# Kernel optimization log

Measured on AMD Instinct MI355X. Metric: run time of the kernel, lower is better.

The kernel has to match this reference:

```python
import jax, jax.numpy as jnp
import numpy as np

B, N, C, H, D, M = 8, 4096, 512, 8, 64, 16
TOPK = 3
TAU = 0.1
DIV_REG = 0.01


def setup_inputs() -> dict:
    key = jax.random.key(0)
    ks = jax.random.split(key, 12)
    w = lambda i, shape: 0.02 * jax.random.normal(ks[i], shape, dtype=jnp.float32)
    return {
        "x": jax.random.normal(ks[0], (B, N, C), dtype=jnp.float32),
        "W_qkv": w(1, (C, 3 * C)),                    # qkv_bias=False
        "W_proj": w(2, (C, C)), "b_proj": jnp.zeros((C,), jnp.float32),
        "W_rspec": w(3, (C, H * M)), "b_rspec": jnp.zeros((H * M,), jnp.float32),
        "W_rspat": w(4, (C, H * M)), "b_rspat": jnp.zeros((H * M,), jnp.float32),
        "K_spec": w(5, (H, M, D)),                    # prototype banks (EMA buffers)
        "K_spat": w(6, (H, M, D)),
        "W_tok": w(7, (D, D)), "b_tok": jnp.zeros((D,), jnp.float32),
        "W_prot": w(8, (D, D)), "b_prot": jnp.zeros((D,), jnp.float32),
    }


def topk_mask_from_logits(logits, k):
    # keep top-k of softmax probs along last axis, renormalize
    vals = jax.lax.top_k(logits, k)[0]
    thresh = vals[..., -1:]
    mask = (logits >= thresh).astype(logits.dtype)
    probs = jax.nn.softmax(logits, axis=-1) * mask
    denom = jnp.maximum(jnp.sum(probs, axis=-1, keepdims=True), 1e-6)
    return probs / denom


def _l2norm(a, eps):
    return a / jnp.maximum(jnp.linalg.norm(a, axis=-1, keepdims=True), eps)


def reference(x, W_qkv, W_proj, b_proj, W_rspec, b_rspec, W_rspat, b_rspat,
              K_spec, K_spat, W_tok, b_tok, W_prot, b_prot):
    # qkv: [B,N,3C] -> q,k,v each [B,H,N,D]
    qkv = (x @ W_qkv).reshape(B, N, 3, H, D).transpose(2, 0, 3, 1, 4)
    q, _k, v = qkv[0], qkv[1], qkv[2]

    # routing logits [B,H,N,M] -> top-k masked probs
    r_spec = topk_mask_from_logits(
        (x @ W_rspec + b_rspec).reshape(B, N, H, M).transpose(0, 2, 1, 3), TOPK)
    r_spat = topk_mask_from_logits(
        (x @ W_rspat + b_rspat).reshape(B, N, H, M).transpose(0, 2, 1, 3), TOPK)

    # effective keys from prototype banks: [B,H,N,D]
    K_eff = (jnp.einsum('bhnm,hmd->bhnd', r_spec, K_spec)
             + jnp.einsum('bhnm,hmd->bhnd', r_spat, K_spat))
    K_norm = jax.nn.softmax(K_eff, axis=-2)          # softmax over tokens N

    # linear attention reorder: context [B,H,D,D], then Q @ context
    context = jnp.einsum('bhnd,bhne->bhde', K_norm, v)
    out = jnp.einsum('bhnd,bhde->bhne', q, context)  # note: scale unused in source
    out = out.transpose(0, 2, 1, 3).reshape(B, N, C) @ W_proj + b_proj

    # ---- contrastive aux loss ----
    t_n = _l2norm(v @ W_tok + b_tok, 1e-12)          # [B,H,N,D]
    p_spec_n = _l2norm(K_spec @ W_prot + b_prot, 1e-12)
    p_spat_n = _l2norm(K_spat @ W_prot + b_prot, 1e-12)
    sim_spec = jnp.einsum('bhnd,hmd->bhnm', t_n, p_spec_n)
    sim_spat = jnp.einsum('bhnd,hmd->bhnm', t_n, p_spat_n)
    pos_spec = jnp.sum(sim_spec * r_spec, axis=-1)
    pos_spat = jnp.sum(sim_spat * r_spat, axis=-1)
    loss_spec = -jnp.mean(pos_spec / TAU - jax.nn.logsumexp(sim_spec / TAU, axis=-1))
    loss_spat = -jnp.mean(pos_spat / TAU - jax.nn.logsumexp(sim_spat / TAU, axis=-1))
    contrastive_loss = 0.5 * (loss_spec + loss_spat)

    def diversity_loss(P):
        h, m, _d = P.shape
        p = P / jnp.maximum(jnp.linalg.norm(P, axis=-1, keepdims=True), 1e-6)
        sim = jnp.einsum('hmd,hnd->hmn', p, p)
        mask = 1.0 - jnp.eye(m, dtype=P.dtype)[None]
        return jnp.sum(sim * mask) / (h * m * (m - 1) + 1e-6)

    diversity = DIV_REG * (diversity_loss(K_spec) + diversity_loss(K_spat))
    return out, contrastive_loss, diversity
```

## Files before the change

kernel.cpp:

```cpp
#include <hip/hip_runtime.h>
#include <math.h>

#define B_ 8
#define N_ 4096
#define C_ 512
#define H_ 8
#define D_ 64
#define M_ 16
#define BN_TOK (B_*N_)
#define TAU_ 0.1f

typedef short s8v __attribute__((ext_vector_type(8)));
typedef float f4v __attribute__((ext_vector_type(4)));
typedef unsigned short u16;

__device__ __forceinline__ float wave_reduce_sum(float v){
  #pragma unroll
  for (int o = 32; o > 0; o >>= 1) v += __shfl_xor(v, o);
  return v;
}

__device__ __forceinline__ unsigned short f2b(float f){
  unsigned int u = __float_as_uint(f);
  u += 0x7fffu + ((u >> 16) & 1u);
  return (unsigned short)(u >> 16);
}

__device__ __forceinline__ float b2f(u16 b){
  return __uint_as_float(((unsigned int)b) << 16);
}

__device__ __forceinline__ s8v pack8(const float* f){
  s8v r;
  #pragma unroll
  for (int e = 0; e < 8; ++e) r[e] = (short)f2b(f[e]);
  return r;
}

__device__ __forceinline__ void gload16(const u16* g, u16* l){
  __builtin_amdgcn_global_load_lds(
      (const __attribute__((address_space(1))) unsigned int*)g,
      (__attribute__((address_space(3))) unsigned int*)l, 16, 0, 0);
}

__global__ __launch_bounds__(256) void prep_all(const float* __restrict__ x, u16* __restrict__ xb,
                                                const float* __restrict__ W_qkv,
                                                const float* __restrict__ W_rspec,
                                                const float* __restrict__ W_rspat,
                                                const float* __restrict__ W_proj,
                                                u16* __restrict__ Wt_qv,
                                                u16* __restrict__ Wt_r,
                                                u16* __restrict__ Wt_p){
  const int bid = blockIdx.x;
  if (bid < 1024) {
    const int n8 = (BN_TOK*C_)/8;
    for (int i = bid * 256 + threadIdx.x; i < n8; i += 1024*256) {
      const float4* p = (const float4*)(x + (size_t)i * 8);
      float4 a = p[0], b = p[1];
      float f[8] = {a.x,a.y,a.z,a.w,b.x,b.y,b.z,b.w};
      *(s8v*)(xb + (size_t)i * 8) = pack8(f);
    }
    return;
  }
  const int r = bid - 1024, k = threadIdx.x;
  const float* src; int ld, coff, n; u16* dst;
  if (r < 512)       { src = W_qkv;   ld = 1536; coff = 0;    n = r;        dst = Wt_qv; }
  else if (r < 1024) { src = W_qkv;   ld = 1536; coff = 1024; n = r - 512;  dst = Wt_qv + 512*512; }
  else if (r < 1152) { src = W_rspec; ld = 128;  coff = 0;    n = r - 1024; dst = Wt_r; }
  else if (r < 1280) { src = W_rspat; ld = 128;  coff = 0;    n = r - 1152; dst = Wt_r + 128*512; }
  else               { src = W_proj;  ld = 512;  coff = 0;    n = r - 1280; dst = Wt_p; }
  dst[(size_t)n*512 + k]       = f2b(src[(size_t)k*ld + coff + n]);
  dst[(size_t)n*512 + k + 256] = f2b(src[(size_t)(k+256)*ld + coff + n]);
}

template<bool OUT_BF16>
__global__ __launch_bounds__(256) void gemm_bt(const u16* __restrict__ A,
                                               const u16* __restrict__ Bt,
                                               const float* __restrict__ bias,
                                               void* __restrict__ C,
                                               int K, int lda, int ldc, int bt_bstride) {
  __shared__ __align__(16) u16 Asm[2][128*32];
  __shared__ __align__(16) u16 Bsm[2][128*32];
  const int tid = threadIdx.x;
  const int lane = tid & 63, w = tid >> 6;
  const int bm = blockIdx.x * 128, bn = blockIdx.y * 128;

  const int lrow = lane >> 2;
  const int kch  = ((lane & 3) ^ ((lane >> 3) & 3)) << 3;

  const u16* Btb = Bt + (size_t)(bm >> 12) * bt_bstride;
  const u16* Ag0 = A   + (size_t)(bm + w*16 + lrow) * lda + kch;
  const u16* Ag1 = Ag0 + (size_t)64 * lda;
  const u16* Bg0 = Btb + (size_t)(bn + w*16 + lrow) * K + kch;
  const u16* Bg1 = Bg0 + (size_t)64 * K;
  const int l0 = (w*16)*32, l1 = (w*16+64)*32;

  const int lm = lane & 15, lg = lane >> 4;
  const int w0 = (w >> 1) * 64, c0 = (w & 1) * 64;
  const int xs = (lg ^ ((lm >> 1) & 3)) << 3;

  f4v acc[4][4];
  #pragma unroll
  for (int i = 0; i < 4; ++i)
    #pragma unroll
    for (int j = 0; j < 4; ++j) acc[i][j] = (f4v){0.f,0.f,0.f,0.f};

  gload16(Ag0, &Asm[0][l0]);
  gload16(Ag1, &Asm[0][l1]);
  gload16(Bg0, &Bsm[0][l0]);
  gload16(Bg1, &Bsm[0][l1]);
  __syncthreads();

  int cur = 0;
  for (int k0 = 0; k0 < K; k0 += 32) {
    const int nxt = cur ^ 1;
    if (k0 + 32 < K) {
      gload16(Ag0 + k0 + 32, &Asm[nxt][l0]);
      gload16(Ag1 + k0 + 32, &Asm[nxt][l1]);
      gload16(Bg0 + k0 + 32, &Bsm[nxt][l0]);
      gload16(Bg1 + k0 + 32, &Bsm[nxt][l1]);
    }
    s8v af[4], bf_[4];
    #pragma unroll
    for (int i = 0; i < 4; ++i) af[i]  = *(const s8v*)&Asm[cur][(w0 + 16*i + lm)*32 + xs];
    #pragma unroll
    for (int j = 0; j < 4; ++j) bf_[j] = *(const s8v*)&Bsm[cur][(c0 + 16*j + lm)*32 + xs];
    #pragma unroll
    for (int i = 0; i < 4; ++i)
      #pragma unroll
      for (int j = 0; j < 4; ++j)
        acc[i][j] = __builtin_amdgcn_mfma_f32_16x16x32_bf16(af[i], bf_[j], acc[i][j], 0, 0, 0);
    __syncthreads();
    cur = nxt;
  }

  #pragma unroll
  for (int j = 0; j < 4; ++j) {
    const int col = bn + c0 + 16*j + lm;
    const float bj = (!OUT_BF16 && bias) ? bias[col] : 0.f;
    #pragma unroll
    for (int i = 0; i < 4; ++i) {
      const int row = bm + w0 + 16*i + 4*lg;
      #pragma unroll
      for (int r = 0; r < 4; ++r) {
        if (OUT_BF16) ((u16*)C)[(size_t)(row + r) * ldc + col] = f2b(acc[i][j][r]);
        else          ((float*)C)[(size_t)(row + r) * ldc + col] = acc[i][j][r] + bj;
      }
    }
  }
}

__global__ __launch_bounds__(256) void router_topk(const float* __restrict__ logits,
                            const float* __restrict__ b_rspec, const float* __restrict__ b_rspat,
                            float* __restrict__ r_spec, float* __restrict__ r_spat,
                            u16* __restrict__ rb_spec, u16* __restrict__ rb_spat) {
  int t = blockIdx.x * blockDim.x + threadIdx.x;
  if (t >= BN_TOK * H_ * 2) return;
  int route = t & 1, h = (t >> 1) & 7, bn = t >> 4;
  int b = bn >> 12, n = bn & 4095;
  const float* lg = logits + (size_t)bn*256 + route*128 + h*16;
  const float* bias = (route ? b_rspat : b_rspec) + h*16;
  float v[16];
  #pragma unroll
  for (int m=0;m<16;++m) v[m] = lg[m] + bias[m];
  float m1=-1e30f, m2=-1e30f, m3=-1e30f;
  #pragma unroll
  for (int m=0;m<16;++m){
    float x=v[m];
    if (x>m1){m3=m2;m2=m1;m1=x;}
    else if (x>m2){m3=m2;m2=x;}
    else if (x>m3){m3=x;}
  }
  float S=0.f, Sm=0.f, e[16];
  #pragma unroll
  for (int m=0;m<16;++m){ e[m]=expf(v[m]-m1); S+=e[m]; if (v[m]>=m3) Sm+=e[m]; }
  float denom = fmaxf(Sm/S, 1e-6f);
  float inv = 1.f/(S*denom);
  size_t idx = (((size_t)b*H_ + h)*N_ + n)*16;
  float* r = (route ? r_spat : r_spec) + idx;
  u16* rb  = (route ? rb_spat : rb_spec) + idx;
  #pragma unroll
  for (int m=0;m<16;++m) {
    float val = (v[m] >= m3) ? e[m]*inv : 0.f;
    r[m] = val;
    rb[m] = f2b(val);
  }
}

__global__ __launch_bounds__(256) void context_mfma(const u16* __restrict__ rb_spec, const u16* __restrict__ rb_spat,
                               const float* __restrict__ K_spec, const float* __restrict__ K_spat,
                               const u16* __restrict__ qvb, float* __restrict__ pctx, float* __restrict__ pZ) {
  const int chunk = blockIdx.x & 15, bh = blockIdx.x >> 4;
  const int b = bh >> 3, h = bh & 7;
  const int tid = threadIdx.x;
  const int lane = tid & 63, w = tid >> 6;
  const int lm = lane & 15, lg = lane >> 4;

  __shared__ __align__(16) unsigned short Kc[64*32];
  __shared__ __align__(16) unsigned short Rs[64*32];
  __shared__ __align__(16) unsigned short Vt[64*64];
  __shared__ __align__(16) unsigned short Ps[64*64];
  __shared__ float Zs[256];

  {
    int d = tid & 63, c = tid >> 6;
    float f[8];
    #pragma unroll
    for (int u = 0; u < 8; ++u) {
      int k = c*8 + u;
      f[u] = (k < 16) ? K_spec[h*1024 + k*64 + d] : K_spat[h*1024 + (k-16)*64 + d];
    }
    *(s8v*)&Kc[d*32 + ((c ^ (d&3)) << 3)] = pack8(f);
  }

  const u16* rsg = rb_spec + ((size_t)bh*N_ + chunk*256)*16;
  const u16* rtg = rb_spat + ((size_t)bh*N_ + chunk*256)*16;
  const u16* vbase = qvb + 512 + h*64;
  const size_t tokbase = (size_t)b*N_ + chunk*256;

  f4v acc2[4];
  #pragma unroll
  for (int j = 0; j < 4; ++j) acc2[j] = (f4v){0.f,0.f,0.f,0.f};
  float zreg[4] = {0.f,0.f,0.f,0.f};

  for (int t0 = 0; t0 < 4; ++t0) {
    __syncthreads();
    {
      int n = tid & 63, c = tid >> 6;
      const u16* src = (c < 2 ? rsg : rtg) + ((size_t)(t0*64 + n))*16 + (c&1)*8;
      *(s8v*)&Rs[n*32 + ((c ^ (n&3)) << 3)] = *(const s8v*)src;
    }
    {
      int n = tid & 63, eq = tid >> 6;
      const u16* src = vbase + (tokbase + t0*64 + n)*1024 + eq*16;
      u16 f[16];
      *(s8v*)&f[0] = ((const s8v*)src)[0];
      *(s8v*)&f[8] = ((const s8v*)src)[1];
      #pragma unroll
      for (int u = 0; u < 16; ++u) {
        int e = eq*16 + u;
        Vt[e*64 + ((((n>>3) ^ (e&7)) << 3) | (n&7))] = f[u];
      }
    }
    __syncthreads();
    {
      s8v a1 = *(const s8v*)&Rs[(16*w + lm)*32 + ((lg ^ (lm&3)) << 3)];
      #pragma unroll
      for (int j = 0; j < 4; ++j) {
        s8v b1 = *(const s8v*)&Kc[(16*j + lm)*32 + ((lg ^ (lm&3)) << 3)];
        f4v c1 = (f4v){0.f,0.f,0.f,0.f};
        c1 = __builtin_amdgcn_mfma_f32_16x16x32_bf16(a1, b1, c1, 0, 0, 0);
        float p0 = expf(c1[0]), p1 = expf(c1[1]), p2 = expf(c1[2]), p3 = expf(c1[3]);
        float zz = p0 + p1 + p2 + p3;
        zz += __shfl_xor(zz, 16); zz += __shfl_xor(zz, 32);
        zreg[j] += zz;
        int d = 16*j + lm;
        int n0w = 16*w + 4*lg;
        Ps[d*64 + (((((n0w  )>>3) ^ (d&7)) << 3) | ((n0w  )&7))] = f2b(p0);
        Ps[d*64 + (((((n0w+1)>>3) ^ (d&7)) << 3) | ((n0w+1)&7))] = f2b(p1);
        Ps[d*64 + (((((n0w+2)>>3) ^ (d&7)) << 3) | ((n0w+2)&7))] = f2b(p2);
        Ps[d*64 + (((((n0w+3)>>3) ^ (d&7)) << 3) | ((n0w+3)&7))] = f2b(p3);
      }
    }
    __syncthreads();
    #pragma unroll
    for (int kb = 0; kb < 2; ++kb) {
      s8v a2 = *(const s8v*)&Vt[(16*w + lm)*64 + (((kb*4 + lg) ^ (lm&7)) << 3)];
      #pragma unroll
      for (int j = 0; j < 4; ++j) {
        s8v b2 = *(const s8v*)&Ps[(16*j + lm)*64 + (((kb*4 + lg) ^ (lm&7)) << 3)];
        acc2[j] = __builtin_amdgcn_mfma_f32_16x16x32_bf16(a2, b2, acc2[j], 0, 0, 0);
      }
    }
  }
  float* pc = pctx + (size_t)(bh*16 + chunk)*4096;
  #pragma unroll
  for (int j = 0; j < 4; ++j) {
    #pragma unroll
    for (int r = 0; r < 4; ++r)
      pc[(16*w + 4*lg + r)*64 + 16*j + lm] = acc2[j][r];
    if (lg == 0) Zs[w*64 + 16*j + lm] = zreg[j];
  }
  __syncthreads();
  if (tid < 64)
    pZ[(size_t)(bh*16 + chunk)*64 + tid] = Zs[tid] + Zs[64+tid] + Zs[128+tid] + Zs[192+tid];
}

__global__ __launch_bounds__(256) void context_reduce(const float* __restrict__ pctx, const float* __restrict__ pZ,
                              float* __restrict__ ctx) {
  const int bh = blockIdx.x;
  const int tid = threadIdx.x;
  const int e = tid >> 2, d0 = (tid & 3) * 16;
  float zs[16];
  #pragma unroll
  for (int j=0;j<16;++j) zs[j]=0.f;
  float s[16];
  #pragma unroll
  for (int j=0;j<16;++j) s[j]=0.f;
  for (int c = 0; c < 16; ++c) {
    const float* zp = pZ + (size_t)(bh*16 + c)*64 + d0;
    #pragma unroll
    for (int j=0;j<16;++j) zs[j] += zp[j];
    const float* pc = pctx + (size_t)(bh*16 + c)*4096 + e*64 + d0;
    #pragma unroll
    for (int j=0;j<16;++j) s[j] += pc[j];
  }
  float* co = ctx + (size_t)bh*4096 + e*64 + d0;
  #pragma unroll
  for (int j=0;j<16;++j) co[j] = s[j] / zs[j];
}

__global__ __launch_bounds__(256) void cwt_kernel(const float* __restrict__ ctx, const u16* __restrict__ Wt_p,
                                                  u16* __restrict__ CWt) {
  const int bh = blockIdx.x >> 3, oct = blockIdx.x & 7;
  const int b = bh >> 3, h = bh & 7;
  const int tid = threadIdx.x;
  __shared__ float ctxS[64*64];
  __shared__ u16 WsL[64*64];
  {
    int e = tid >> 2, dq = tid & 3;
    const float4* src = (const float4*)(ctx + (size_t)bh*4096 + e*64 + dq*16);
    float4* dst = (float4*)(ctxS + e*64 + dq*16);
    dst[0] = src[0]; dst[1] = src[1]; dst[2] = src[2]; dst[3] = src[3];
  }
  const int c0 = oct * 64;
  {
    int cl = tid >> 2, eq = tid & 3;
    const s8v* src = (const s8v*)(Wt_p + (size_t)(c0 + cl)*512 + h*64 + eq*16);
    *(s8v*)&WsL[cl*64 + eq*16]     = src[0];
    *(s8v*)&WsL[cl*64 + eq*16 + 8] = src[1];
  }
  __syncthreads();
  const int d = tid & 63, cq = tid >> 6;
  for (int ci = 0; ci < 16; ++ci) {
    int cl = cq*16 + ci;
    float acc = 0.f;
    #pragma unroll
    for (int e = 0; e < 64; ++e)
      acc = fmaf(ctxS[e*64 + d], b2f(WsL[cl*64 + e]), acc);
    CWt[((size_t)b*512 + (c0 + cl))*512 + h*64 + d] = f2b(acc);
  }
}

__global__ __launch_bounds__(64) void protnorm_div(const float* __restrict__ K_spec, const float* __restrict__ K_spat,
                               const float* __restrict__ W_prot, const float* __restrict__ b_prot,
                               float* __restrict__ pnorm, float* __restrict__ pdiv) {
  const int bid = blockIdx.x;
  const int e = threadIdx.x;
  if (bid < 256) {
    int route = bid >> 7, hm = bid & 127;
    const float* Km = (route ? K_spat : K_spec) + hm*64;
    __shared__ float kv[64];
    kv[e] = Km[e];
    __syncthreads();
    float acc = b_prot[e];
    for (int dcol = 0; dcol < 64; ++dcol) acc = fmaf(kv[dcol], W_prot[dcol*64 + e], acc);
    float n2 = wave_reduce_sum(acc*acc);
    pnorm[(size_t)bid*64 + e] = acc / fmaxf(sqrtf(n2), 1e-12f);
    return;
  }
  const int db = bid - 256;
  int route = db >> 3, h = db & 7;
  const float* Km = (route ? K_spat : K_spec) + h*16*64;
  float s = 0.f, selfsum = 0.f;
  for (int m = 0; m < 16; ++m) {
    float x = Km[m*64 + e];
    float n2 = wave_reduce_sum(x*x);
    float p = x / fmaxf(sqrtf(n2), 1e-6f);
    s += p; selfsum += p*p;
  }
  float off = wave_reduce_sum(s*s - selfsum);
  if (e == 0) pdiv[db] = off;
}

__global__ __launch_bounds__(256) void contrastive_mfma(const u16* __restrict__ qvb,
                                   const float* __restrict__ r_spec, const float* __restrict__ r_spat,
                                   const float* __restrict__ W_tok, const float* __restrict__ b_tok,
                                   const float* __restrict__ pnorm, float* __restrict__ pcontr) {
  const int tile = blockIdx.x & 255;
  const int h = blockIdx.x >> 8;
  const int t0 = tile * 128;
  const int b = t0 >> 12;
  const int n0 = t0 & 4095;
  const int tid = threadIdx.x;
  const int lane = tid & 63, w = tid >> 6;
  const int lm = lane & 15, lg = lane >> 4;

  __shared__ __align__(16) unsigned short Usm[128*72];
  __shared__ __align__(16) unsigned short Wsm[64*72];
  __shared__ __align__(16) unsigned short Psm[32*72];
  __shared__ float nrmS[128];
  __shared__ float btkS[64];
  __shared__ float bred[2][4];
  float* Uf = (float*)Usm;

  {
    const int vr = tid >> 1, vh = tid & 1;
    const u16* vg = qvb + (size_t)(b*N_ + n0 + vr)*1024 + 512 + h*64 + vh*32;
    #pragma unroll
    for (int c = 0; c < 4; ++c) *(s8v*)&Usm[vr*72 + vh*32 + c*8] = ((const s8v*)vg)[c];
  }
  {
    const int e = tid & 63, kh = tid >> 6;
    float f[16];
    #pragma unroll
    for (int rr = 0; rr < 16; ++rr) f[rr] = W_tok[(size_t)(kh*16+rr)*64 + e];
    *(s8v*)&Wsm[e*72 + kh*16]     = pack8(&f[0]);
    *(s8v*)&Wsm[e*72 + kh*16 + 8] = pack8(&f[8]);
  }
  if (tid < 128) {
    const int proto = tid >> 2, q4 = tid & 3;
    const int src = (proto < 16) ? (h*16 + proto) : (128 + h*16 + (proto-16));
    const float* pg = pnorm + (size_t)src*64 + q4*16;
    float f[16];
    #pragma unroll
    for (int i = 0; i < 4; ++i) {
      float4 v4 = ((const float4*)pg)[i];
      f[4*i]=v4.x; f[4*i+1]=v4.y; f[4*i+2]=v4.z; f[4*i+3]=v4.w;
    }
    *(s8v*)&Psm[proto*72 + q4*16]     = pack8(&f[0]);
    *(s8v*)&Psm[proto*72 + q4*16 + 8] = pack8(&f[8]);
  }
  if (tid < 64) btkS[tid] = b_tok[tid];
  __syncthreads();

  f4v acc[2][4];
  #pragma unroll
  for (int i=0;i<2;++i)
    #pragma unroll
    for (int j=0;j<4;++j) acc[i][j] = (f4v){0.f,0.f,0.f,0.f};
  {
    s8v bf0[4], bf1[4];
    #pragma unroll
    for (int j=0;j<4;++j) {
      bf0[j] = *(const s8v*)&Wsm[(j*16+lm)*72 + lg*8];
      bf1[j] = *(const s8v*)&Wsm[(j*16+lm)*72 + 32 + lg*8];
    }
    #pragma unroll
    for (int i=0;i<2;++i) {
      s8v af0 = *(const s8v*)&Usm[(w*32+16*i+lm)*72 + lg*8];
      s8v af1 = *(const s8v*)&Usm[(w*32+16*i+lm)*72 + 32 + lg*8];
      #pragma unroll
      for (int j=0;j<4;++j) {
        acc[i][j] = __builtin_amdgcn_mfma_f32_16x16x32_bf16(af0, bf0[j], acc[i][j], 0, 0, 0);
        acc[i][j] = __builtin_amdgcn_mfma_f32_16x16x32_bf16(af1, bf1[j], acc[i][j], 0, 0, 0);
      }
    }
  }
  #pragma unroll
  for (int i=0;i<2;++i) {
    #pragma unroll
    for (int r=0;r<4;++r) {
      float s = 0.f;
      #pragma unroll
      for (int j=0;j<4;++j) {
        float val = acc[i][j][r] + btkS[j*16+lm];
        acc[i][j][r] = val;
        s += val*val;
      }
      s += __shfl_xor(s,1); s += __shfl_xor(s,2); s += __shfl_xor(s,4); s += __shfl_xor(s,8);
      if (lm == 0) nrmS[w*32 + 16*i + lg*4 + r] = s;
    }
  }
  #pragma unroll
  for (int i=0;i<2;++i)
    #pragma unroll
    for (int j=0;j<4;++j)
      #pragma unroll
      for (int r=0;r<4;++r)
        Usm[(w*32+16*i+lg*4+r)*72 + j*16+lm] = f2b(acc[i][j][r]);
  __syncthreads();

  f4v acc2[2][2];
  #pragma unroll
  for (int i=0;i<2;++i)
    #pragma unroll
    for (int j=0;j<2;++j) acc2[i][j] = (f4v){0.f,0.f,0.f,0.f};
  {
    s8v bf0[2], bf1[2];
    #pragma unroll
    for (int j=0;j<2;++j) {
      bf0[j] = *(const s8v*)&Psm[(j*16+lm)*72 + lg*8];
      bf1[j] = *(const s8v*)&Psm[(j*16+lm)*72 + 32 + lg*8];
    }
    #pragma unroll
    for (int i=0;i<2;++i) {
      s8v af0 = *(const s8v*)&Usm[(w*32+16*i+lm)*72 + lg*8];
      s8v af1 = *(const s8v*)&Usm[(w*32+16*i+lm)*72 + 32 + lg*8];
      #pragma unroll
      for (int j=0;j<2;++j) {
        acc2[i][j] = __builtin_amdgcn_mfma_f32_16x16x32_bf16(af0, bf0[j], acc2[i][j], 0, 0, 0);
        acc2[i][j] = __builtin_amdgcn_mfma_f32_16x16x32_bf16(af1, bf1[j], acc2[i][j], 0, 0, 0);
      }
    }
  }
  #pragma unroll
  for (int i=0;i<2;++i)
    #pragma unroll
    for (int j=0;j<2;++j)
      #pragma unroll
      for (int r=0;r<4;++r)
        Uf[(w*32+16*i+lg*4+r)*36 + j*16+lm] = acc2[i][j][r];
  __syncthreads();

  float l = 0.f;
  {
    const int tt = tid >> 1, route = tid & 1;
    float inv = 1.f / fmaxf(sqrtf(nrmS[tt]), 1e-12f);
    const float* rg = (route ? r_spat : r_spec) + (((size_t)b*H_ + h)*N_ + n0 + tt)*16;
    float s0[16];
    #pragma unroll
    for (int m=0;m<16;++m) s0[m] = Uf[tt*36 + route*16 + m]*inv;
    float pos = 0.f, mx = -1e30f;
    #pragma unroll
    for (int m=0;m<16;++m) {
      pos += s0[m]*rg[m];
      mx = fmaxf(mx, s0[m]);
    }
    float z = 0.f;
    #pragma unroll
    for (int m=0;m<16;++m) z += expf((s0[m]-mx)/TAU_);
    l = pos/TAU_ - (mx/TAU_ + logf(z));
  }
  float lspec = (tid & 1) ? 0.f : l;
  float lspat = (tid & 1) ? l : 0.f;
  lspec = wave_reduce_sum(lspec);
  lspat = wave_reduce_sum(lspat);
  if (lane == 0) { bred[0][w]=lspec; bred[1][w]=lspat; }
  __syncthreads();
  if (tid == 0) {
    pcontr[2*blockIdx.x]     = bred[0][0]+bred[0][1]+bred[0][2]+bred[0][3];
    pcontr[2*blockIdx.x + 1] = bred[1][0]+bred[1][1]+bred[1][2]+bred[1][3];
  }
}

__global__ __launch_bounds__(256) void finalize_kernel(const float* __restrict__ pcontr,
                                                       const float* __restrict__ pdiv,
                                                       float* __restrict__ tail) {
  __shared__ float red[2][4];
  const int tid = threadIdx.x, lane = tid & 63, w = tid >> 6;
  float ls = 0.f, lt = 0.f;
  for (int k = tid; k < 2048; k += 256) { ls += pcontr[2*k]; lt += pcontr[2*k + 1]; }
  ls = wave_reduce_sum(ls);
  lt = wave_reduce_sum(lt);
  if (lane == 0) { red[0][w] = ls; red[1][w] = lt; }
  __syncthreads();
  if (tid == 0) {
    float sspec = red[0][0]+red[0][1]+red[0][2]+red[0][3];
    float sspat = red[1][0]+red[1][1]+red[1][2]+red[1][3];
    float dspec = 0.f, dspat = 0.f;
    for (int k = 0; k < 8; ++k) { dspec += pdiv[k]; dspat += pdiv[8+k]; }
    float loss_spec = -(sspec / (float)(B_*H_*N_));
    float loss_spat = -(sspat / (float)(B_*H_*N_));
    float denom = (float)(H_*M_*(M_-1)) + 1e-6f;
    tail[0] = 0.5f*(loss_spec + loss_spat);
    tail[1] = 0.01f * (dspec/denom + dspat/denom);
  }
}

extern "C" void kernel_launch(void* const* d_in, const int* in_sizes, int n_in,
                              void* d_out, int out_size, void* d_ws, size_t ws_size,
                              hipStream_t stream) {
  const float* x       = (const float*)d_in[0];
  const float* W_qkv   = (const float*)d_in[1];
  const float* W_proj  = (const float*)d_in[2];
  const float* b_proj  = (const float*)d_in[3];
  const float* W_rspec = (const float*)d_in[4];
  const float* b_rspec = (const float*)d_in[5];
  const float* W_rspat = (const float*)d_in[6];
  const float* b_rspat = (const float*)d_in[7];
  const float* K_spec  = (const float*)d_in[8];
  const float* K_spat  = (const float*)d_in[9];
  const float* W_tok   = (const float*)d_in[10];
  const float* b_tok   = (const float*)d_in[11];
  const float* W_prot  = (const float*)d_in[12];
  const float* b_prot  = (const float*)d_in[13];
  float* out = (float*)d_out;

  float* ws = (float*)d_ws;
  u16*   qvb     = (u16*)ws;
  float* logits  = ws + 16777216;
  float* pctx    = ws + 16777216;
  float* pZ      = ws + 16777216 + 4194304;
  float* r_spec  = ws + 25165824;
  float* r_spat  = ws + 29360128;
  u16*   rb_spec = (u16*)(ws + 33554432);
  u16*   rb_spat = (u16*)(ws + 35651584);
  u16*   xb      = (u16*)(ws + 37748736);
  u16*   Wt_qv   = (u16*)(ws + 46137344);
  u16*   Wt_r    = (u16*)(ws + 46399488);
  u16*   Wt_p    = (u16*)(ws + 46465024);
  float* ctxb    = ws + 46596096;
  float* pnorm   = ws + 46858240;
  float* pcontr  = ws + 46874624;
  float* pdiv    = ws + 46878720;
  u16*   CWt     = (u16*)(ws + 46878736);

  dim3 blk256(256);

  prep_all<<<2816, blk256, 0, stream>>>(x, xb, W_qkv, W_rspec, W_rspat, W_proj, Wt_qv, Wt_r, Wt_p);

  gemm_bt<false><<<dim3(256,2), blk256, 0, stream>>>(xb, Wt_r, nullptr, logits, 512, 512, 256, 0);
  router_topk<<<2048, blk256, 0, stream>>>(logits, b_rspec, b_rspat, r_spec, r_spat, rb_spec, rb_spat);
  gemm_bt<true><<<dim3(256,8), blk256, 0, stream>>>(xb, Wt_qv, nullptr, qvb, 512, 512, 1024, 0);
  context_mfma<<<1024, blk256, 0, stream>>>(rb_spec, rb_spat, K_spec, K_spat, qvb, pctx, pZ);
  context_reduce<<<64, blk256, 0, stream>>>(pctx, pZ, ctxb);
  cwt_kernel<<<512, blk256, 0, stream>>>(ctxb, Wt_p, CWt);
  protnorm_div<<<272, dim3(64), 0, stream>>>(K_spec, K_spat, W_prot, b_prot, pnorm, pdiv);
  contrastive_mfma<<<2048, blk256, 0, stream>>>(qvb, r_spec, r_spat, W_tok, b_tok, pnorm, pcontr);
  gemm_bt<false><<<dim3(256,4), blk256, 0, stream>>>(qvb, CWt, b_proj, out, 512, 1024, 512, 512*512);
  finalize_kernel<<<1, blk256, 0, stream>>>(pcontr, pdiv, out + 16777216);
}
```

Before: 353.2 us.

## Triple-buffer GEMM shared-memory tiles with explicit vmcnt waits

```diff
diff --git a/kernel.cpp b/kernel.cpp
--- a/kernel.cpp
+++ b/kernel.cpp
@@ -79,8 +79,8 @@
                                                const float* __restrict__ bias,
                                                void* __restrict__ C,
                                                int K, int lda, int ldc, int bt_bstride) {
-  __shared__ __align__(16) u16 Asm[2][128*32];
-  __shared__ __align__(16) u16 Bsm[2][128*32];
+  __shared__ __align__(16) u16 Asm[3][128*32];
+  __shared__ __align__(16) u16 Bsm[3][128*32];
   const int tid = threadIdx.x;
   const int lane = tid & 63, w = tid >> 6;
   const int bm = blockIdx.x * 128, bn = blockIdx.y * 128;
@@ -99,27 +99,30 @@
   const int w0 = (w >> 1) * 64, c0 = (w & 1) * 64;
   const int xs = (lg ^ ((lm >> 1) & 3)) << 3;
 
+  const int NSTEP = K >> 5;
+
   f4v acc[4][4];
   #pragma unroll
   for (int i = 0; i < 4; ++i)
     #pragma unroll
     for (int j = 0; j < 4; ++j) acc[i][j] = (f4v){0.f,0.f,0.f,0.f};
 
-  gload16(Ag0, &Asm[0][l0]);
-  gload16(Ag1, &Asm[0][l1]);
-  gload16(Bg0, &Bsm[0][l0]);
-  gload16(Bg1, &Bsm[0][l1]);
-  __syncthreads();
+  #pragma unroll
+  for (int t = 0; t < 3; ++t) {
+    gload16(Ag0 + t*32, &Asm[t][l0]);
+    gload16(Ag1 + t*32, &Asm[t][l1]);
+    gload16(Bg0 + t*32, &Bsm[t][l0]);
+    gload16(Bg1 + t*32, &Bsm[t][l1]);
+  }
 
   int cur = 0;
-  for (int k0 = 0; k0 < K; k0 += 32) {
-    const int nxt = cur ^ 1;
-    if (k0 + 32 < K) {
-      gload16(Ag0 + k0 + 32, &Asm[nxt][l0]);
-      gload16(Ag1 + k0 + 32, &Asm[nxt][l1]);
-      gload16(Bg0 + k0 + 32, &Bsm[nxt][l0]);
-      gload16(Bg1 + k0 + 32, &Bsm[nxt][l1]);
-    }
+  for (int k = 0; k < NSTEP; ++k) {
+    if (k < NSTEP - 2)       asm volatile("s_waitcnt vmcnt(8)" ::: "memory");
+    else if (k == NSTEP - 2) asm volatile("s_waitcnt vmcnt(4)" ::: "memory");
+    else                     asm volatile("s_waitcnt vmcnt(0)" ::: "memory");
+    __builtin_amdgcn_s_barrier();
+    __builtin_amdgcn_sched_barrier(0);
+
     s8v af[4], bf_[4];
     #pragma unroll
     for (int i = 0; i < 4; ++i) af[i]  = *(const s8v*)&Asm[cur][(w0 + 16*i + lm)*32 + xs];
@@ -130,8 +133,17 @@
       #pragma unroll
       for (int j = 0; j < 4; ++j)
         acc[i][j] = __builtin_amdgcn_mfma_f32_16x16x32_bf16(af[i], bf_[j], acc[i][j], 0, 0, 0);
-    __syncthreads();
-    cur = nxt;
+
+    __builtin_amdgcn_sched_barrier(0);
+    __builtin_amdgcn_s_barrier();
+    if (k + 3 < NSTEP) {
+      gload16(Ag0 + (k+3)*32, &Asm[cur][l0]);
+      gload16(Ag1 + (k+3)*32, &Asm[cur][l1]);
+      gload16(Bg0 + (k+3)*32, &Bsm[cur][l0]);
+      gload16(Bg1 + (k+3)*32, &Bsm[cur][l1]);
+    }
+    __builtin_amdgcn_sched_barrier(0);
+    cur = (cur == 2) ? 0 : cur + 1;
   }
 
   #pragma unroll
```

After: 345.2 us. 1.02x faster.
